# Kernel tuning notes

Measured on AMD Instinct MI355X. Metric: run time of the kernel, lower is better.

The kernel has to match this reference:

```python
import jax, jax.numpy as jnp
import numpy as np
import math

B, S, D = 2, 2048, 2048
HQ, HKV = 16, 4            # query heads, kv heads
HD = D // HQ               # head dim = 128
REPS = HQ // HKV           # queries per kv head = 4
KVD = HKV * HD             # 512


def setup_inputs() -> dict:
    key = jax.random.key(0)
    ks = jax.random.split(key, 7)
    s = 0.02
    return {
        "hidden_states": jax.random.normal(ks[0], (B, S, D), dtype=jnp.float32),
        "Wq": jax.random.normal(ks[1], (D, D), dtype=jnp.float32) * s,
        "bq": jnp.zeros((D,), dtype=jnp.float32),
        "Wk": jax.random.normal(ks[2], (D, KVD), dtype=jnp.float32) * s,
        "bk": jnp.zeros((KVD,), dtype=jnp.float32),
        "Wv": jax.random.normal(ks[3], (D, KVD), dtype=jnp.float32) * s,
        "bv": jnp.zeros((KVD,), dtype=jnp.float32),
    }


def reference(hidden_states, Wq, bq, Wk, bk, Wv, bv):
    b, s, d = hidden_states.shape
    # Projections
    q = hidden_states @ Wq + bq                      # [B,S,D]
    k = hidden_states @ Wk + bk                      # [B,S,KVD]
    v = hidden_states @ Wv + bv                      # [B,S,KVD]
    # Split heads. torch repeat_kv_heads uses .repeat (tile), so expanded
    # head h maps to kv head (h mod HKV). Reshape q heads as (REPS, HKV)
    # so axis g indexes the kv head, matching that tiling exactly.
    q = q.reshape(b, s, HQ, HD).transpose(0, 2, 1, 3)          # [B,HQ,S,hd]
    q = q.reshape(b, REPS, HKV, s, HD)                          # [B,R,G,S,hd]
    k = k.reshape(b, s, HKV, HD).transpose(0, 2, 1, 3)          # [B,G,S,hd]
    v = v.reshape(b, s, HKV, HD).transpose(0, 2, 1, 3)          # [B,G,S,hd]
    scale = 1.0 / math.sqrt(HD)
    scores = jnp.einsum('brgsd,bgtd->brgst', q, k) * scale      # [B,R,G,S,S]
    probs = jax.nn.softmax(scores, axis=-1)
    ctx = jnp.einsum('brgst,bgtd->brgsd', probs, v)             # [B,R,G,S,hd]
    ctx = ctx.reshape(b, HQ, s, HD).transpose(0, 2, 1, 3)       # [B,S,HQ,hd]
    return ctx.reshape(b, s, HQ * HD)                            # [B,S,D]
```

## Files before the change

kernel.cpp:

```cpp
#include <hip/hip_runtime.h>
#include <hip/hip_bf16.h>

#define QSCALE   0.08838834764831845f
#define QKSCALE  0.1275174468755322f

typedef __attribute__((ext_vector_type(8))) short bh8;
typedef __attribute__((ext_vector_type(4))) float fx4;
typedef __attribute__((ext_vector_type(4))) short sh4;

typedef const __attribute__((address_space(1))) unsigned GAu;
typedef __attribute__((address_space(3))) unsigned LAu;

__device__ __forceinline__ short f2bf(float f) {
    unsigned u = __float_as_uint(f);
    unsigned r = u + 0x7fffu + ((u >> 16) & 1u);
    return (short)(r >> 16);
}

__device__ __forceinline__ unsigned pk_bf16(float x, float y) {
    union { __hip_bfloat162 h; unsigned u; } cv;
    cv.h = __float22bfloat162_rn(float2{x, y});
    return cv.u;
}

__global__ __launch_bounds__(256) void prep_all(
    const float* __restrict__ x,  short* __restrict__ xo,
    const float* __restrict__ wq, short* __restrict__ wqt,
    const float* __restrict__ wk, short* __restrict__ wkt,
    const float* __restrict__ wv, short* __restrict__ wvt) {
    __shared__ float tile[32][33];
    const int bid = blockIdx.x;

    if (bid < 8192) {
        int i = bid * 256 + threadIdx.x;
        float4 v = ((const float4*)x)[i];
        sh4 s;
        s.x = f2bf(v.x); s.y = f2bf(v.y); s.z = f2bf(v.z); s.w = f2bf(v.w);
        ((sh4*)xo)[i] = s;
        return;
    }

    const float* w; short* wt; int K, N, nb, kb;
    int t = bid - 8192;
    if (t < 4096)      { w = wq; wt = wqt; K = 2048; N = 2048; nb = t & 63; kb = t >> 6; }
    else if (t < 5120) { w = wk; wt = wkt; K = 2048; N = 512;  t -= 4096; nb = t & 15; kb = t >> 4; }
    else               { w = wv; wt = wvt; K = 2048; N = 512;  t -= 5120; nb = t & 15; kb = t >> 4; }

    int tx = threadIdx.x & 31, ty = threadIdx.x >> 5;
#pragma unroll
    for (int j = 0; j < 4; ++j) {
        int k = kb * 32 + ty + j * 8;
        tile[ty + j * 8][tx] = w[(size_t)k * N + nb * 32 + tx];
    }
    __syncthreads();
#pragma unroll
    for (int j = 0; j < 4; ++j) {
        int n = nb * 32 + ty + j * 8;
        wt[(size_t)n * K + kb * 32 + tx] = f2bf(tile[tx][ty + j * 8]);
    }
}

__global__ __launch_bounds__(256) void proj_gemm(
    const short* __restrict__ X,
    const short* __restrict__ WqT,
    const short* __restrict__ WkT,
    const short* __restrict__ WvT,
    const float* __restrict__ bq, const float* __restrict__ bk,
    const float* __restrict__ bv,
    short* __restrict__ Qb, short* __restrict__ Kpk, short* __restrict__ Vpk) {
    __shared__ short As0[128 * 32];
    __shared__ short As1[128 * 32];
    __shared__ short Bs0[128 * 32];
    __shared__ short Bs1[128 * 32];

    const int tid = threadIdx.x;
    const int bm = blockIdx.x;
    const int ntg = blockIdx.y;

    const short* Wm; const float* bias; int col0, kind;
    if (ntg < 16)      { Wm = WqT; bias = bq; col0 = ntg * 128;        kind = 0; }
    else if (ntg < 20) { Wm = WkT; bias = bk; col0 = (ntg - 16) * 128; kind = 1; }
    else               { Wm = WvT; bias = bv; col0 = (ntg - 20) * 128; kind = 2; }

    const int w = tid >> 6, lane = tid & 63, quad = lane >> 4, l16 = lane & 15;

    fx4 acc[2][8];
#pragma unroll
    for (int i = 0; i < 2; ++i)
#pragma unroll
        for (int j = 0; j < 8; ++j) acc[i][j] = fx4{0.f, 0.f, 0.f, 0.f};

    const int srow = w * 16 + (lane >> 2);
    const int scol = (((lane & 3) ^ ((lane >> 2) & 3)) * 8);
    const short* Ag = X + (size_t)(bm * 128 + srow) * 2048 + scol;
    const short* Bg = Wm + (size_t)(col0 + srow) * 2048 + scol;
    const int stoff = w * 512;

    const int fchunk = (quad ^ (l16 & 3)) * 8;
    const int aoff0 = (w * 32 + l16) * 32 + fchunk;
    const int aoff1 = aoff0 + 512;
    const int boff  = l16 * 32 + fchunk;

    const short* pA00 = As0 + aoff0;  const short* pA01 = As0 + aoff1;
    const short* pA10 = As1 + aoff0;  const short* pA11 = As1 + aoff1;
    const short* pB0  = Bs0 + boff;   const short* pB1  = Bs1 + boff;

#define PG_STAGE(AsD, BsD, ktile)                                               \
    do {                                                                        \
        const int k0_ = (ktile) * 32;                                           \
        _Pragma("unroll")                                                       \
        for (int j = 0; j < 2; ++j) {                                           \
            __builtin_amdgcn_global_load_lds(                                   \
                (GAu*)(Ag + (size_t)(j * 64) * 2048 + k0_),                     \
                (LAu*)(AsD + stoff + j * 2048), 16, 0, 0);                      \
            __builtin_amdgcn_global_load_lds(                                   \
                (GAu*)(Bg + (size_t)(j * 64) * 2048 + k0_),                     \
                (LAu*)(BsD + stoff + j * 2048), 16, 0, 0);                      \
        }                                                                       \
    } while (0)

#define PG_COMPUTE(pA0_, pA1_, pB_)                                             \
    do {                                                                        \
        bh8 af0 = *(const bh8*)(pA0_);                                          \
        bh8 af1 = *(const bh8*)(pA1_);                                          \
        _Pragma("unroll")                                                       \
        for (int nt = 0; nt < 8; ++nt) {                                        \
            bh8 bf = *(const bh8*)((pB_) + nt * 512);                           \
            acc[0][nt] = __builtin_amdgcn_mfma_f32_16x16x32_bf16(af0, bf, acc[0][nt], 0, 0, 0); \
            acc[1][nt] = __builtin_amdgcn_mfma_f32_16x16x32_bf16(af1, bf, acc[1][nt], 0, 0, 0); \
        }                                                                       \
    } while (0)

    PG_STAGE(As0, Bs0, 0);
    __syncthreads();

    for (int kt = 0; kt < 64; kt += 2) {
        PG_STAGE(As1, Bs1, kt + 1);
        PG_COMPUTE(pA00, pA01, pB0);
        __syncthreads();

        if (kt < 62) PG_STAGE(As0, Bs0, kt + 2);
        PG_COMPUTE(pA10, pA11, pB1);
        __syncthreads();
    }
#undef PG_STAGE
#undef PG_COMPUTE

#pragma unroll
    for (int mt = 0; mt < 2; ++mt) {
        int srow2 = bm * 128 + w * 32 + mt * 16 + quad * 4;
#pragma unroll
        for (int nt = 0; nt < 8; ++nt) {
            int c = col0 + nt * 16 + l16;
            float bval = bias[c];
#pragma unroll
            for (int r = 0; r < 4; ++r) {
                int sg = srow2 + r;
                int b = sg >> 11, s = sg & 2047;
                float v = acc[mt][nt][r] + bval;
                int hd = c & 127;
                if (kind == 0) {
                    v *= QKSCALE;
                    int h = c >> 7;
                    Qb[(((size_t)(b * 16 + h) * 2048 + s) << 7) + hd] = f2bf(v);
                } else if (kind == 1) {
                    int g = c >> 7;
                    int kt32 = s >> 5, u = s & 31;
                    int nti = (u >> 2) & 1, fl16 = (u >> 3) * 4 + (u & 3);
                    int ks = hd >> 5, qd = (hd >> 3) & 3, j = hd & 7;
                    size_t frag = (((size_t)(b * 4 + g) * 64 + kt32) * 8 + nti * 4 + ks);
                    Kpk[frag * 512 + (qd * 16 + fl16) * 8 + j] = f2bf(v);
                } else {
                    int g = c >> 7;
                    int ktt = s >> 6, tl = s & 63;
                    int ts = tl >> 5, qd = (tl >> 3) & 3, j = tl & 7;
                    int fnt = hd >> 4, fl16 = hd & 15;
                    size_t frag = (((size_t)(b * 4 + g) * 32 + ktt) * 16 + fnt * 2 + ts);
                    Vpk[frag * 512 + (qd * 16 + fl16) * 8 + j] = f2bf(v);
                }
            }
        }
    }
}

__global__ __launch_bounds__(128, 2) void attn(
    const short* __restrict__ Qb,
    const short* __restrict__ Kpk,
    const short* __restrict__ Vpk,
    float* __restrict__ out) {
    __shared__ short Ks0[8 * 512];
    __shared__ short Ks1[8 * 512];
    __shared__ short Vs0[8 * 512];
    __shared__ short Vs1[8 * 512];

    const int bid = blockIdx.x;
    const int gb = bid & 7;
    const int rep = (bid >> 3) & 3;
    const int qt = bid >> 5;
    const int b = gb >> 2, g = gb & 3;
    const int h = rep * 4 + g;
    const int tid = threadIdx.x, w = tid >> 6, lane = tid & 63;
    const int quad = lane >> 4, l16 = lane & 15;

    bh8 qf[2][4];
#pragma unroll
    for (int rg = 0; rg < 2; ++rg) {
        int s = qt * 64 + w * 32 + rg * 16 + l16;
        const short* qp = Qb + (((size_t)(b * 16 + h) * 2048 + s) << 7);
#pragma unroll
        for (int ks = 0; ks < 4; ++ks)
            qf[rg][ks] = *(const bh8*)(qp + ks * 32 + quad * 8);
    }

    const short* kbase = Kpk + ((size_t)gb * 32) * 8192;
    const short* vbase = Vpk + ((size_t)gb * 32) * 8192;

    const short* pK0 = Ks0 + lane * 8;
    const short* pK1 = Ks1 + lane * 8;
    const short* pV0 = Vs0 + lane * 8;
    const short* pV1 = Vs1 + lane * 8;

    fx4 ctx[2][8];
#pragma unroll
    for (int rg = 0; rg < 2; ++rg)
#pragma unroll
        for (int j = 0; j < 8; ++j) ctx[rg][j] = fx4{0.f, 0.f, 0.f, 0.f};
    float l_part[2] = {0.f, 0.f};

#define AT_BARRIER()  asm volatile("s_waitcnt lgkmcnt(0)\n\ts_barrier" ::: "memory")
#define AT_VM(N)      asm volatile("s_waitcnt vmcnt(" #N ")" ::: "memory")

#define AT_STAGE(KsD, VsD, kn)                                                  \
    do {                                                                        \
        const short* kp_ = kbase + (size_t)(kn) * 4096;                         \
        const short* vp_ = vbase + (size_t)((kn) >> 1) * 8192 + ((kn) & 1) * 512;\
        _Pragma("unroll")                                                       \
        for (int i = 0; i < 4; ++i) {                                           \
            int f = w * 4 + i;                                                  \
            __builtin_amdgcn_global_load_lds((GAu*)(kp_ + f * 512 + lane * 8),  \
                                             (LAu*)(KsD + f * 512), 16, 0, 0);  \
            __builtin_amdgcn_global_load_lds((GAu*)(vp_ + (size_t)f * 1024 + lane * 8),\
                                             (LAu*)(VsD + f * 512), 16, 0, 0);  \
        }                                                                       \
    } while (0)

#define AT_COMPUTE(pKC, pVC)                                                    \
    do {                                                                        \
        fx4 sc[2][2];                                                           \
        sc[0][0] = fx4{0.f, 0.f, 0.f, 0.f}; sc[0][1] = fx4{0.f, 0.f, 0.f, 0.f}; \
        sc[1][0] = fx4{0.f, 0.f, 0.f, 0.f}; sc[1][1] = fx4{0.f, 0.f, 0.f, 0.f}; \
        __builtin_amdgcn_s_setprio(1);                                          \
        _Pragma("unroll")                                                       \
        for (int nti = 0; nti < 2; ++nti) {                                     \
            _Pragma("unroll")                                                   \
            for (int ks = 0; ks < 4; ++ks) {                                    \
                bh8 kf = *(const bh8*)((pKC) + (nti * 4 + ks) * 512);           \
                sc[0][nti] = __builtin_amdgcn_mfma_f32_16x16x32_bf16(kf, qf[0][ks], sc[0][nti], 0, 0, 0); \
                sc[1][nti] = __builtin_amdgcn_mfma_f32_16x16x32_bf16(kf, qf[1][ks], sc[1][nti], 0, 0, 0); \
            }                                                                   \
        }                                                                       \
        __builtin_amdgcn_s_setprio(0);                                          \
        bh8 pa[2];                                                              \
        _Pragma("unroll")                                                       \
        for (int rg = 0; rg < 2; ++rg) {                                        \
            float e0 = __builtin_amdgcn_exp2f(sc[rg][0][0]);                    \
            float e1 = __builtin_amdgcn_exp2f(sc[rg][0][1]);                    \
            float e2 = __builtin_amdgcn_exp2f(sc[rg][0][2]);                    \
            float e3 = __builtin_amdgcn_exp2f(sc[rg][0][3]);                    \
            float e4 = __builtin_amdgcn_exp2f(sc[rg][1][0]);                    \
            float e5 = __builtin_amdgcn_exp2f(sc[rg][1][1]);                    \
            float e6 = __builtin_amdgcn_exp2f(sc[rg][1][2]);                    \
            float e7 = __builtin_amdgcn_exp2f(sc[rg][1][3]);                    \
            l_part[rg] += ((e0 + e1) + (e2 + e3)) + ((e4 + e5) + (e6 + e7));    \
            unsigned a[4];                                                      \
            a[0] = pk_bf16(e0, e1);                                             \
            a[1] = pk_bf16(e2, e3);                                             \
            a[2] = pk_bf16(e4, e5);                                             \
            a[3] = pk_bf16(e6, e7);                                             \
            pa[rg] = *(const bh8*)a;                                            \
        }                                                                       \
        __builtin_amdgcn_s_setprio(1);                                          \
        _Pragma("unroll")                                                       \
        for (int nt = 0; nt < 8; ++nt) {                                        \
            bh8 vf = *(const bh8*)((pVC) + nt * 512);                           \
            ctx[0][nt] = __builtin_amdgcn_mfma_f32_16x16x32_bf16(pa[0], vf, ctx[0][nt], 0, 0, 0); \
            ctx[1][nt] = __builtin_amdgcn_mfma_f32_16x16x32_bf16(pa[1], vf, ctx[1][nt], 0, 0, 0); \
        }                                                                       \
        __builtin_amdgcn_s_setprio(0);                                          \
    } while (0)

    AT_STAGE(Ks0, Vs0, 0);
    AT_STAGE(Ks1, Vs1, 1);
    AT_VM(0);
    AT_BARRIER();

    for (int kt = 0; kt < 62; kt += 2) {
        AT_COMPUTE(pK0, pV0);
        AT_BARRIER();
        AT_STAGE(Ks0, Vs0, kt + 2);
        AT_VM(8);
        AT_BARRIER();
        AT_COMPUTE(pK1, pV1);
        AT_BARRIER();
        AT_STAGE(Ks1, Vs1, kt + 3);
        AT_VM(8);
        AT_BARRIER();
    }
    AT_COMPUTE(pK0, pV0);
    AT_VM(0);
    AT_BARRIER();
    AT_COMPUTE(pK1, pV1);
#undef AT_STAGE
#undef AT_COMPUTE
#undef AT_BARRIER
#undef AT_VM

#pragma unroll
    for (int rg = 0; rg < 2; ++rg) {
        float lsum = l_part[rg];
        lsum += __shfl_xor(lsum, 16);
        lsum += __shfl_xor(lsum, 32);
        int srow = qt * 64 + w * 32 + rg * 16 + quad * 4;
#pragma unroll
        for (int r = 0; r < 4; ++r) {
            float inv = 1.f / __shfl(lsum, quad * 4 + r);
            size_t rowoff = ((size_t)b * 2048 + (srow + r)) * 2048 + h * 128;
#pragma unroll
            for (int nt = 0; nt < 8; ++nt)
                out[rowoff + nt * 16 + l16] = ctx[rg][nt][r] * inv;
        }
    }
}

extern "C" void kernel_launch(void* const* d_in, const int* in_sizes, int n_in,
                              void* d_out, int out_size, void* d_ws, size_t ws_size,
                              hipStream_t stream) {
    const float* hs = (const float*)d_in[0];
    const float* Wq = (const float*)d_in[1];
    const float* bq = (const float*)d_in[2];
    const float* Wk = (const float*)d_in[3];
    const float* bk = (const float*)d_in[4];
    const float* Wv = (const float*)d_in[5];
    const float* bv = (const float*)d_in[6];
    float* out = (float*)d_out;

    char* ws = (char*)d_ws;
    short* Xbf = (short*)(ws);
    short* WqT = (short*)(ws + 16777216);
    short* WkT = (short*)(ws + 25165824);
    short* WvT = (short*)(ws + 27262976);
    short* Qb  = (short*)(ws + 29360128);
    short* Kpk = (short*)(ws + 46137344);
    short* Vpk = (short*)(ws + 50331648);

    prep_all<<<14336, 256, 0, stream>>>(hs, Xbf, Wq, WqT, Wk, WkT, Wv, WvT);
    proj_gemm<<<dim3(32, 24), 256, 0, stream>>>(Xbf, WqT, WkT, WvT, bq, bk, bv,
                                                Qb, Kpk, Vpk);
    attn<<<1024, 128, 0, stream>>>(Qb, Kpk, Vpk, out);
}
```

Before: 260.9 us.

## Load K/V fragments directly from global into registers, dropping LDS staging

Replaces the double-buffered LDS staging of K and V tiles (global_load_lds plus barriers) with direct per-wave global loads into registers. K fragments for the next tile are prefetched into a second register set while the current tile computes. This removes barriers and LDS traffic, but the two waves of a block now each fetch the same K/V data from global/L2 separately. It also raises register pressure, which may affect occupancy at launch bounds of 2 blocks per CU.

```diff
diff --git a/kernel.cpp b/kernel.cpp
--- a/kernel.cpp
+++ b/kernel.cpp
@@ -188,11 +188,6 @@
     const short* __restrict__ Kpk,
     const short* __restrict__ Vpk,
     float* __restrict__ out) {
-    __shared__ short Ks0[8 * 512];
-    __shared__ short Ks1[8 * 512];
-    __shared__ short Vs0[8 * 512];
-    __shared__ short Vs1[8 * 512];
-
     const int bid = blockIdx.x;
     const int gb = bid & 7;
     const int rep = (bid >> 3) & 3;
@@ -212,13 +207,8 @@
             qf[rg][ks] = *(const bh8*)(qp + ks * 32 + quad * 8);
     }
 
-    const short* kbase = Kpk + ((size_t)gb * 32) * 8192;
-    const short* vbase = Vpk + ((size_t)gb * 32) * 8192;
-
-    const short* pK0 = Ks0 + lane * 8;
-    const short* pK1 = Ks1 + lane * 8;
-    const short* pV0 = Vs0 + lane * 8;
-    const short* pV1 = Vs1 + lane * 8;
+    const short* kbase = Kpk + ((size_t)gb * 32) * 8192 + lane * 8;
+    const short* vbase = Vpk + ((size_t)gb * 32) * 8192 + lane * 8;
 
     fx4 ctx[2][8];
 #pragma unroll
@@ -227,24 +217,7 @@
         for (int j = 0; j < 8; ++j) ctx[rg][j] = fx4{0.f, 0.f, 0.f, 0.f};
     float l_part[2] = {0.f, 0.f};
 
-#define AT_BARRIER()  asm volatile("s_waitcnt lgkmcnt(0)\n\ts_barrier" ::: "memory")
-#define AT_VM(N)      asm volatile("s_waitcnt vmcnt(" #N ")" ::: "memory")
-
-#define AT_STAGE(KsD, VsD, kn)                                                  \
-    do {                                                                        \
-        const short* kp_ = kbase + (size_t)(kn) * 4096;                         \
-        const short* vp_ = vbase + (size_t)((kn) >> 1) * 8192 + ((kn) & 1) * 512;\
-        _Pragma("unroll")                                                       \
-        for (int i = 0; i < 4; ++i) {                                           \
-            int f = w * 4 + i;                                                  \
-            __builtin_amdgcn_global_load_lds((GAu*)(kp_ + f * 512 + lane * 8),  \
-                                             (LAu*)(KsD + f * 512), 16, 0, 0);  \
-            __builtin_amdgcn_global_load_lds((GAu*)(vp_ + (size_t)f * 1024 + lane * 8),\
-                                             (LAu*)(VsD + f * 512), 16, 0, 0);  \
-        }                                                                       \
-    } while (0)
-
-#define AT_COMPUTE(pKC, pVC)                                                    \
+#define AT_COMPUTE(kX, vf)                                                      \
     do {                                                                        \
         fx4 sc[2][2];                                                           \
         sc[0][0] = fx4{0.f, 0.f, 0.f, 0.f}; sc[0][1] = fx4{0.f, 0.f, 0.f, 0.f}; \
@@ -254,9 +227,8 @@
         for (int nti = 0; nti < 2; ++nti) {                                     \
             _Pragma("unroll")                                                   \
             for (int ks = 0; ks < 4; ++ks) {                                    \
-                bh8 kf = *(const bh8*)((pKC) + (nti * 4 + ks) * 512);           \
-                sc[0][nti] = __builtin_amdgcn_mfma_f32_16x16x32_bf16(kf, qf[0][ks], sc[0][nti], 0, 0, 0); \
-                sc[1][nti] = __builtin_amdgcn_mfma_f32_16x16x32_bf16(kf, qf[1][ks], sc[1][nti], 0, 0, 0); \
+                sc[0][nti] = __builtin_amdgcn_mfma_f32_16x16x32_bf16(kX[nti * 4 + ks], qf[0][ks], sc[0][nti], 0, 0, 0); \
+                sc[1][nti] = __builtin_amdgcn_mfma_f32_16x16x32_bf16(kX[nti * 4 + ks], qf[1][ks], sc[1][nti], 0, 0, 0); \
             }                                                                   \
         }                                                                       \
         __builtin_amdgcn_s_setprio(0);                                          \
@@ -282,38 +254,46 @@
         __builtin_amdgcn_s_setprio(1);                                          \
         _Pragma("unroll")                                                       \
         for (int nt = 0; nt < 8; ++nt) {                                        \
-            bh8 vf = *(const bh8*)((pVC) + nt * 512);                           \
-            ctx[0][nt] = __builtin_amdgcn_mfma_f32_16x16x32_bf16(pa[0], vf, ctx[0][nt], 0, 0, 0); \
-            ctx[1][nt] = __builtin_amdgcn_mfma_f32_16x16x32_bf16(pa[1], vf, ctx[1][nt], 0, 0, 0); \
+            ctx[0][nt] = __builtin_amdgcn_mfma_f32_16x16x32_bf16(pa[0], vf[nt], ctx[0][nt], 0, 0, 0); \
+            ctx[1][nt] = __builtin_amdgcn_mfma_f32_16x16x32_bf16(pa[1], vf[nt], ctx[1][nt], 0, 0, 0); \
         }                                                                       \
         __builtin_amdgcn_s_setprio(0);                                          \
     } while (0)
 
-    AT_STAGE(Ks0, Vs0, 0);
-    AT_STAGE(Ks1, Vs1, 1);
-    AT_VM(0);
-    AT_BARRIER();
-
-    for (int kt = 0; kt < 62; kt += 2) {
-        AT_COMPUTE(pK0, pV0);
-        AT_BARRIER();
-        AT_STAGE(Ks0, Vs0, kt + 2);
-        AT_VM(8);
-        AT_BARRIER();
-        AT_COMPUTE(pK1, pV1);
-        AT_BARRIER();
-        AT_STAGE(Ks1, Vs1, kt + 3);
-        AT_VM(8);
-        AT_BARRIER();
-    }
-    AT_COMPUTE(pK0, pV0);
-    AT_VM(0);
-    AT_BARRIER();
-    AT_COMPUTE(pK1, pV1);
-#undef AT_STAGE
+    bh8 kA[8], kB[8];
+#pragma unroll
+    for (int f = 0; f < 8; ++f)
+        kA[f] = *(const bh8*)(kbase + f * 512);
+
+    for (int kt = 0; kt < 64; kt += 2) {
+        {
+            const short* vp = vbase + (size_t)(kt >> 1) * 8192;
+            bh8 vf[8];
+#pragma unroll
+            for (int nt = 0; nt < 8; ++nt)
+                vf[nt] = *(const bh8*)(vp + nt * 1024);
+            const short* kp = kbase + (size_t)(kt + 1) * 4096;
+#pragma unroll
+            for (int f = 0; f < 8; ++f)
+                kB[f] = *(const bh8*)(kp + f * 512);
+            AT_COMPUTE(kA, vf);
+        }
+        {
+            const short* vp = vbase + (size_t)(kt >> 1) * 8192 + 512;
+            bh8 vf[8];
+#pragma unroll
+            for (int nt = 0; nt < 8; ++nt)
+                vf[nt] = *(const bh8*)(vp + nt * 1024);
+            if (kt < 62) {
+                const short* kp = kbase + (size_t)(kt + 2) * 4096;
+#pragma unroll
+                for (int f = 0; f < 8; ++f)
+                    kA[f] = *(const bh8*)(kp + f * 512);
+            }
+            AT_COMPUTE(kB, vf);
+        }
+    }
 #undef AT_COMPUTE
-#undef AT_BARRIER
-#undef AT_VM
 
 #pragma unroll
     for (int rg = 0; rg < 2; ++rg) {
```

After: 265.7 us. About the same (+1.8%).
